# Kernel tuning notes

Measured on AMD Instinct MI355X. Metric: run time of the kernel, lower is better.

## Reference

```python
import jax, jax.numpy as jnp
import numpy as np

N = 8192
FEAT = 200
SEG = FEAT // 4  # 50
OUT = 300


def setup_inputs() -> dict:
    key = jax.random.key(0)
    ks = jax.random.split(key, 10)
    x = jax.random.normal(ks[0], (N, FEAT), dtype=jnp.float32)
    # row-normalized-ish dense adjacencies so activations stay O(1)
    A_S = jax.random.uniform(ks[1], (N, N), dtype=jnp.float32) / N
    A_F = jax.random.uniform(ks[2], (N, N), dtype=jnp.float32) / N
    gcn_W = jax.random.normal(ks[3], (SEG, SEG), dtype=jnp.float32) / np.sqrt(SEG)
    gcn_b = jnp.zeros((SEG,), dtype=jnp.float32)
    # 12 forget gates: order s1,s2,s3,f1,f2,f3,s1b,s2b,s3b,f1b,f2b,f3b
    gates_W = jax.random.normal(ks[4], (12, 2 * SEG, SEG), dtype=jnp.float32)
    gates_b = jax.random.normal(ks[5], (12, SEG), dtype=jnp.float32)
    proj_W = jax.random.normal(ks[6], (8 * SEG, OUT), dtype=jnp.float32) / np.sqrt(8 * SEG)
    proj_b = jnp.zeros((OUT,), dtype=jnp.float32)
    return {"x": x, "A_S": A_S, "A_F": A_F, "gcn_W": gcn_W, "gcn_b": gcn_b,
            "gates_W": gates_W, "gates_b": gates_b, "proj_W": proj_W, "proj_b": proj_b}


def _lgfm(x, A_S, A_F, gcn_W, gcn_b, gates_W, gates_b, proj_W, proj_b):
    seg = x.shape[1] // 4

    def gcn(h, A):
        # Kipf GraphConvolution: relu(A @ (h @ W) + b); dropout inactive (eval)
        return jax.nn.relu(A @ (h @ gcn_W) + gcn_b)

    def gate(i, h1, h2):
        a = jax.nn.sigmoid(jnp.concatenate([h1, h2], axis=1) @ gates_W[i] + gates_b[i])
        return a * h1

    GS1, GS2, GS3, GF1, GF2, GF3 = 0, 1, 2, 3, 4, 5
    GS1B, GS2B, GS3B, GF1B, GF2B, GF3B = 6, 7, 8, 9, 10, 11

    x1, x2, x3, x4 = x[:, :seg], x[:, seg:2 * seg], x[:, 2 * seg:3 * seg], x[:, 3 * seg:]

    # forward branch (F path then S gating)
    t1_XF1 = x1 + gcn(x1, A_F)
    t1_XS1 = gcn(x1, A_S)
    t1_XF2 = 0.2 * t1_XS1 + 0.8 * gcn(t1_XF1, A_F)
    t2_XF1 = x2 + gcn(x2, A_F)
    t2_XS1 = gcn(x2, A_S)
    t2_XS1 = t2_XS1 + gate(GS1, t1_XS1, t2_XS1)
    t2_XF2 = 0.2 * t2_XS1 + 0.8 * gcn(t2_XF1, A_F)
    t2_XF2 = gate(GF1, t1_XF2, t2_XF2) + t2_XF2
    t3_XF1 = 0.2 * x3 + 0.8 * gcn(x3, A_F)
    t3_XS1 = gcn(x3, A_S)
    t3_XS1 = t3_XS1 + gate(GS2, t2_XS1, t3_XS1)
    t3_XF2 = 0.2 * t3_XS1 + 0.8 * gcn(t3_XF1, A_F)
    t3_XF2 = gate(GF2, t2_XF2, t3_XF2) + t3_XF2
    t4_XF1 = x4 + gcn(x4, A_F)
    t4_XS1 = gcn(x4, A_S)
    t4_XS1 = t4_XS1 + gate(GS3, t3_XS1, t4_XS1)
    t4_XF2 = 0.2 * t4_XS1 + 0.8 * gcn(t4_XF1, A_F)
    t4_XF2 = gate(GF3, t3_XF2, t4_XF2) + t4_XF2

    # mirrored branch (S path then F gating)
    t1_XS1b = x1 + gcn(x1, A_S)
    t1_XF1b = gcn(x1, A_F)
    t1_XS2 = 0.2 * t1_XF1b + 0.8 * gcn(t1_XS1b, A_S)
    t2_XS1b = x2 + gcn(x2, A_S)
    t2_XF1b = gcn(x2, A_F)
    t2_XF1b = t2_XF1b + gate(GF1B, t1_XF1b, t2_XF1b)
    t2_XS2 = 0.2 * t2_XF1b + 0.8 * gcn(t2_XS1b, A_S)
    t2_XS2 = gate(GS1B, t1_XS2, t2_XS2) + t2_XS2
    t3_XS1b = 0.2 * x3 + 0.8 * gcn(x3, A_S)
    t3_XF1b = gcn(x3, A_F)
    t3_XF1b = t3_XF1b + gate(GF2B, t2_XF1b, t3_XF1b)
    t3_XS2 = 0.2 * t3_XF1b + 0.8 * gcn(t3_XS1b, A_S)
    t3_XS2 = gate(GS2B, t2_XS2, t3_XS2) + t3_XS2
    t4_XS1b = x4 + gcn(x4, A_S)
    t4_XF1b = gcn(x4, A_F)
    t4_XF1b = t4_XF1b + gate(GF3B, t3_XF1b, t4_XF1b)
    t4_XS2 = 0.2 * t4_XF1b + 0.8 * gcn(t4_XS1b, A_S)
    t4_XS2 = gate(GS3B, t3_XS2, t4_XS2) + t4_XS2

    h_L = jnp.concatenate([t1_XF2, t1_XS2, t2_XF2, t2_XS2,
                           t3_XF2, t3_XS2, t4_XF2, t4_XS2], axis=1)
    return h_L @ proj_W + proj_b


def reference(x, A_S, A_F, gcn_W, gcn_b, gates_W, gates_b, proj_W, proj_b):
    return _lgfm(x, A_S, A_F, gcn_W, gcn_b, gates_W, gates_b, proj_W, proj_b)
```

## Files before the change

kernel.cpp:

```cpp
#include <hip/hip_runtime.h>
#include <math.h>

typedef float float4v __attribute__((ext_vector_type(4)));
typedef __attribute__((ext_vector_type(4))) float f32x4;
typedef __attribute__((ext_vector_type(8))) short short8v;
typedef __attribute__((ext_vector_type(8))) unsigned short ushort8v;

#define NROW 8192
#define FEAT 200
#define OUTC 300
#define ZLD  256
#define HLK  448
#define HLN  384

__device__ __forceinline__ unsigned short f2bf(float x) {
  unsigned u = __float_as_uint(x);
  return (unsigned short)((u + 0x7fffu + ((u >> 16) & 1u)) >> 16);
}

__global__ __launch_bounds__(256) void zmul_t_kernel(
    const float* __restrict__ x, const float* __restrict__ W,
    unsigned short* __restrict__ Zt) {
  __shared__ float Ws[2500];
  __shared__ float hs[16][200];
  __shared__ float zbuf[16][256];
  int t = threadIdx.x;
  int r0 = blockIdx.x * 16;
  for (int i = t; i < 2500; i += 256) Ws[i] = W[i];
  for (int i = t; i < 16 * FEAT; i += 256)
    hs[0][i] = x[(size_t)r0 * FEAT + i];
  __syncthreads();
  for (int i = t; i < 16 * 256; i += 256) {
    int row = i >> 8, j = i & 255;
    float acc = 0.f;
    if (j < FEAT) {
      int s = j / 50, jj = j % 50;
      const float* hrow = &hs[row][s * 50];
      #pragma unroll 5
      for (int k = 0; k < 50; ++k) acc += hrow[k] * Ws[k * 50 + jj];
    }
    zbuf[row][j] = acc;
  }
  __syncthreads();
  unsigned int* Ztu = (unsigned int*)Zt;
  for (int i = t; i < 256 * 8; i += 256) {
    int j = i >> 3, w2 = i & 7;
    unsigned int lo = f2bf(zbuf[2 * w2][j]);
    unsigned int hi = f2bf(zbuf[2 * w2 + 1][j]);
    Ztu[((j * NROW + r0) >> 1) + w2] = lo | (hi << 16);
  }
}

__global__ __launch_bounds__(256, 2) void gemm_cvt_pair_kernel(
    const float* __restrict__ AF, const float* __restrict__ AS,
    const unsigned short* __restrict__ ZtF,
    const unsigned short* __restrict__ ZtS,
    float* __restrict__ Cpart) {
  int d = blockIdx.x;
  int L = (d & 7) * 64 + (d >> 3);
  int mat = L & 1;
  int ks  = (L >> 1) & 1;
  int cb  = (L >> 2) & 1;
  int rb  = L >> 3;

  const float* __restrict__ A = mat ? AS : AF;
  const unsigned short* __restrict__ Zt = mat ? ZtS : ZtF;

  int t = threadIdx.x;
  int lane = t & 63, wv = t >> 6;
  int row0 = rb * 128, n0 = cb * 128, k0 = ks * 4096;

  __shared__ short As[2][128 * 64];
  __shared__ short Bs[2][128 * 64];

  int srcAf[4], dstA[4];
  #pragma unroll
  for (int i = 0; i < 4; ++i) {
    int cc = i * 256 + t;
    int m = cc >> 3, s = cc & 7;
    srcAf[i] = (row0 + m) * NROW + s * 8;
    dstA[i] = m * 64 + ((s ^ (m & 7)) * 8);
  }
  int srcB[4], ldsDstB[4];
  #pragma unroll
  for (int i = 0; i < 4; ++i) {
    int c = i * 256 + t;
    int m = c >> 3, sl = c & 7;
    srcB[i] = (n0 + m) * NROW + ((sl ^ (m & 7)) * 8);
    ldsDstB[i] = (i * 256 + wv * 64) * 8;
  }

  f32x4 ar0[4], ar1[4];

#define STAGE_B(buf, kt)                                                              \
  {                                                                                   \
    _Pragma("unroll")                                                                 \
    for (int i = 0; i < 4; ++i)                                                       \
      __builtin_amdgcn_global_load_lds(                                               \
          (const __attribute__((address_space(1))) void*)(Zt + srcB[i] + (kt)),       \
          (__attribute__((address_space(3))) void*)(&Bs[buf][ldsDstB[i]]), 16, 0, 0); \
  }
#define LOAD_A(kt)                                         \
  {                                                        \
    _Pragma("unroll")                                      \
    for (int i = 0; i < 4; ++i) {                          \
      ar0[i] = *(const f32x4*)&A[srcAf[i] + (kt)];         \
      ar1[i] = *(const f32x4*)&A[srcAf[i] + (kt) + 4];     \
    }                                                      \
  }
#define WRITE_A(buf)                                                                    \
  {                                                                                     \
    _Pragma("unroll")                                                                   \
    for (int i = 0; i < 4; ++i) {                                                       \
      unsigned u0_, u1_, u2_, u3_;                                                      \
      asm("v_cvt_pk_bf16_f32 %0, %1, %2" : "=v"(u0_) : "v"(ar0[i][0]), "v"(ar0[i][1]));\
      asm("v_cvt_pk_bf16_f32 %0, %1, %2" : "=v"(u1_) : "v"(ar0[i][2]), "v"(ar0[i][3]));\
      asm("v_cvt_pk_bf16_f32 %0, %1, %2" : "=v"(u2_) : "v"(ar1[i][0]), "v"(ar1[i][1]));\
      asm("v_cvt_pk_bf16_f32 %0, %1, %2" : "=v"(u3_) : "v"(ar1[i][2]), "v"(ar1[i][3]));\
      union { unsigned u[4]; short8v v; } pk_;                                          \
      pk_.u[0] = u0_; pk_.u[1] = u1_; pk_.u[2] = u2_; pk_.u[3] = u3_;                   \
      *(short8v*)&As[buf][dstA[i]] = pk_.v;                                             \
    }                                                                                   \
  }

  f32x4 acc[4][4];
  #pragma unroll
  for (int i = 0; i < 4; ++i)
    #pragma unroll
    for (int j = 0; j < 4; ++j) acc[i][j] = (f32x4)0.f;

  int m0 = (wv >> 1) * 64, n0w = (wv & 1) * 64;
  int l15 = lane & 15, l4 = lane >> 4;

  int cur = 0;
  LOAD_A(k0)
  STAGE_B(0, k0)
  WRITE_A(0)
  __syncthreads();

  for (int it = 0; it < 64; ++it) {
    if (it + 1 < 64) {
      STAGE_B(cur ^ 1, k0 + (it + 1) * 64)
      LOAD_A(k0 + (it + 1) * 64)
    }

    #pragma unroll
    for (int kk = 0; kk < 2; ++kk) {
      int slot = kk * 4 + l4;
      short8v a[4], b[4];
      #pragma unroll
      for (int i = 0; i < 4; ++i) {
        int m = m0 + i * 16 + l15;
        a[i] = *(const short8v*)&As[cur][m * 64 + ((slot ^ (m & 7)) * 8)];
        int n = n0w + i * 16 + l15;
        b[i] = *(const short8v*)&Bs[cur][n * 64 + ((slot ^ (n & 7)) * 8)];
      }
      #pragma unroll
      for (int i = 0; i < 4; ++i)
        #pragma unroll
        for (int j = 0; j < 4; ++j)
          acc[i][j] = __builtin_amdgcn_mfma_f32_16x16x32_bf16(a[i], b[j], acc[i][j], 0, 0, 0);
    }

    if (it + 1 < 64) WRITE_A(cur ^ 1)
    __syncthreads();
    cur ^= 1;
  }
#undef STAGE_B
#undef LOAD_A
#undef WRITE_A

  int s = mat * 2 + ks;
  #pragma unroll
  for (int i = 0; i < 4; ++i) {
    #pragma unroll
    for (int j = 0; j < 4; ++j) {
      int c = n0 + n0w + j * 16 + l15;
      #pragma unroll
      for (int q = 0; q < 4; ++q) {
        int r = row0 + m0 + i * 16 + l4 * 4 + q;
        Cpart[((size_t)(s * NROW + r) << 8) + c] = acc[i][j][q];
      }
    }
  }
}

__global__ __launch_bounds__(256) void reduce_zmul_kernel(
    const float* __restrict__ Cpart, const float* __restrict__ bias,
    const float* __restrict__ x, const float* __restrict__ W,
    float* __restrict__ GF0, float* __restrict__ GS0,
    unsigned short* __restrict__ ZtF, unsigned short* __restrict__ ZtS) {
  __shared__ float Ws[2500];
  __shared__ float hs[16][200];
  __shared__ float zbuf[16][256];
  int t = threadIdx.x;
  int r0 = blockIdx.x * 16;
  int w = t >> 6, j = t & 63;
  bool act = j < 50;
  int rbase = r0 + w * 4;
  for (int i = t; i < 2500; i += 256) Ws[i] = W[i];

  const float alpha[4] = {1.f, 1.f, 0.2f, 1.f};
  const float beta[4]  = {1.f, 1.f, 0.8f, 1.f};
  float gf[4][4], gs[4][4];
  if (act) {
    float bv = bias[j];
    #pragma unroll
    for (int r = 0; r < 4; ++r)
      #pragma unroll
      for (int s = 0; s < 4; ++s) {
        int c = s * 50 + j;
        size_t base = (((size_t)(rbase + r)) << 8) + c;
        float vF = Cpart[base] + Cpart[base + (size_t)NROW * 256];
        float vS = Cpart[base + (size_t)2 * NROW * 256] + Cpart[base + (size_t)3 * NROW * 256];
        gf[r][s] = fmaxf(vF + bv, 0.f);
        gs[r][s] = fmaxf(vS + bv, 0.f);
        GF0[(size_t)(rbase + r) * FEAT + c] = gf[r][s];
        GS0[(size_t)(rbase + r) * FEAT + c] = gs[r][s];
      }
    #pragma unroll
    for (int r = 0; r < 4; ++r)
      #pragma unroll
      for (int s = 0; s < 4; ++s)
        hs[w * 4 + r][s * 50 + j] =
            alpha[s] * x[(size_t)(rbase + r) * FEAT + s * 50 + j] + beta[s] * gf[r][s];
  }
  __syncthreads();
  for (int i = t; i < 16 * 256; i += 256) {
    int row = i >> 8, jj = i & 255;
    float acc = 0.f;
    if (jj < FEAT) {
      int s = jj / 50, j2 = jj % 50;
      const float* hrow = &hs[row][s * 50];
      #pragma unroll 5
      for (int k = 0; k < 50; ++k) acc += hrow[k] * Ws[k * 50 + j2];
    }
    zbuf[row][jj] = acc;
  }
  __syncthreads();
  {
    unsigned int* Ztu = (unsigned int*)ZtF;
    for (int i = t; i < 256 * 8; i += 256) {
      int j2 = i >> 3, w2 = i & 7;
      unsigned int lo = f2bf(zbuf[2 * w2][j2]);
      unsigned int hi = f2bf(zbuf[2 * w2 + 1][j2]);
      Ztu[((j2 * NROW + r0) >> 1) + w2] = lo | (hi << 16);
    }
  }
  if (act) {
    #pragma unroll
    for (int r = 0; r < 4; ++r)
      #pragma unroll
      for (int s = 0; s < 4; ++s)
        hs[w * 4 + r][s * 50 + j] =
            alpha[s] * x[(size_t)(rbase + r) * FEAT + s * 50 + j] + beta[s] * gs[r][s];
  }
  __syncthreads();
  for (int i = t; i < 16 * 256; i += 256) {
    int row = i >> 8, jj = i & 255;
    float acc = 0.f;
    if (jj < FEAT) {
      int s = jj / 50, j2 = jj % 50;
      const float* hrow = &hs[row][s * 50];
      #pragma unroll 5
      for (int k = 0; k < 50; ++k) acc += hrow[k] * Ws[k * 50 + j2];
    }
    zbuf[row][jj] = acc;
  }
  __syncthreads();
  {
    unsigned int* Ztu = (unsigned int*)ZtS;
    for (int i = t; i < 256 * 8; i += 256) {
      int j2 = i >> 3, w2 = i & 7;
      unsigned int lo = f2bf(zbuf[2 * w2][j2]);
      unsigned int hi = f2bf(zbuf[2 * w2 + 1][j2]);
      Ztu[((j2 * NROW + r0) >> 1) + w2] = lo | (hi << 16);
    }
  }
}

__device__ __forceinline__ void gate4(const float* __restrict__ gWi, const float* __restrict__ gbi,
                                      float* hsw, float* Wg, int t, int j, bool act,
                                      const float* h1, const float* h2, float* aout) {
  if (act) {
    #pragma unroll
    for (int r = 0; r < 4; ++r) { hsw[r * 128 + j] = h1[r]; hsw[r * 128 + 64 + j] = h2[r]; }
  }
  {
    const float4v* src = (const float4v*)gWi;
    float4v* dst = (float4v*)Wg;
    #pragma unroll
    for (int u = 0; u < 5; ++u) {
      int i = t + 256 * u;
      if (i < 1250) dst[i] = src[i];
    }
  }
  __syncthreads();
  float acc0 = 0.f, acc1 = 0.f, acc2 = 0.f, acc3 = 0.f;
  if (act) {
    float bv = gbi[j];
    acc0 = bv; acc1 = bv; acc2 = bv; acc3 = bv;
    #pragma unroll 2
    for (int k = 0; k < 50; ++k) {
      float wv = Wg[k * 50 + j];
      acc0 += hsw[0 * 128 + k] * wv;
      acc1 += hsw[1 * 128 + k] * wv;
      acc2 += hsw[2 * 128 + k] * wv;
      acc3 += hsw[3 * 128 + k] * wv;
    }
    #pragma unroll 2
    for (int k = 0; k < 50; ++k) {
      float wv = Wg[(50 + k) * 50 + j];
      acc0 += hsw[0 * 128 + 64 + k] * wv;
      acc1 += hsw[1 * 128 + 64 + k] * wv;
      acc2 += hsw[2 * 128 + 64 + k] * wv;
      acc3 += hsw[3 * 128 + 64 + k] * wv;
    }
  }
  __syncthreads();
  float accs[4] = {acc0, acc1, acc2, acc3};
  #pragma unroll
  for (int r = 0; r < 4; ++r) {
    float a = 1.f / (1.f + expf(-accs[r]));
    aout[r] = a * h1[r];
  }
}

__global__ __launch_bounds__(256) void reduce_chain_kernel(
    const float* __restrict__ Cpart, const float* __restrict__ bias,
    const float* __restrict__ GF0, const float* __restrict__ GS0,
    const float* __restrict__ gW, const float* __restrict__ gb,
    unsigned short* __restrict__ hLb) {
  __shared__ float hsb[4 * 512];
  __shared__ float Wg[5000];
  int t = threadIdx.x;
  int w = t >> 6, j = t & 63;
  bool act = j < 50;
  float* hsw = &hsb[w * 512];
  int rbase = blockIdx.x * 16 + w * 4;

  float gf0[4][4], gs0[4][4], gf1[4][4], gs1[4][4];
  if (act) {
    float bv = bias[j];
    #pragma unroll
    for (int r = 0; r < 4; ++r)
      #pragma unroll
      for (int s = 0; s < 4; ++s) {
        int c = s * 50 + j;
        size_t base = (((size_t)(rbase + r)) << 8) + c;
        float vF = Cpart[base] + Cpart[base + (size_t)NROW * 256];
        float vS = Cpart[base + (size_t)2 * NROW * 256] + Cpart[base + (size_t)3 * NROW * 256];
        gf1[r][s] = fmaxf(vF + bv, 0.f);
        gs1[r][s] = fmaxf(vS + bv, 0.f);
        gf0[r][s] = GF0[(size_t)(rbase + r) * FEAT + c];
        gs0[r][s] = GS0[(size_t)(rbase + r) * FEAT + c];
      }
  }
  if (!act) {
    for (int p = j - 50; p < 48; p += 14)
      #pragma unroll
      for (int r = 0; r < 4; ++r)
        hLb[(size_t)(rbase + r) * HLK + 400 + p] = 0;
  }

  float xf2[4], xs1[4], pre[4], a[4], h1t[4], h2t[4];
  #pragma unroll
  for (int r = 0; r < 4; ++r) xf2[r] = 0.2f * gs0[r][0] + 0.8f * gf1[r][0];
  if (act) {
    #pragma unroll
    for (int r = 0; r < 4; ++r) hLb[(size_t)(rbase + r) * HLK + 0 + j] = f2bf(xf2[r]);
  }
  #pragma unroll
  for (int r = 0; r < 4; ++r) { h1t[r] = gs0[r][0]; h2t[r] = gs0[r][1]; }
  gate4(gW + 0 * 5000, gb + 0 * 50, hsw, Wg, t, j, act, h1t, h2t, a);
  #pragma unroll
  for (int r = 0; r < 4; ++r) xs1[r] = gs0[r][1] + a[r];
  #pragma unroll
  for (int r = 0; r < 4; ++r) pre[r] = 0.2f * xs1[r] + 0.8f * gf1[r][1];
  gate4(gW + 3 * 5000, gb + 3 * 50, hsw, Wg, t, j, act, xf2, pre, a);
  #pragma unroll
  for (int r = 0; r < 4; ++r) xf2[r] = a[r] + pre[r];
  if (act) {
    #pragma unroll
    for (int r = 0; r < 4; ++r) hLb[(size_t)(rbase + r) * HLK + 100 + j] = f2bf(xf2[r]);
  }
  #pragma unroll
  for (int r = 0; r < 4; ++r) { h1t[r] = xs1[r]; h2t[r] = gs0[r][2]; }
  gate4(gW + 1 * 5000, gb + 1 * 50, hsw, Wg, t, j, act, h1t, h2t, a);
  #pragma unroll
  for (int r = 0; r < 4; ++r) xs1[r] = gs0[r][2] + a[r];
  #pragma unroll
  for (int r = 0; r < 4; ++r) pre[r] = 0.2f * xs1[r] + 0.8f * gf1[r][2];
  gate4(gW + 4 * 5000, gb + 4 * 50, hsw, Wg, t, j, act, xf2, pre, a);
  #pragma unroll
  for (int r = 0; r < 4; ++r) xf2[r] = a[r] + pre[r];
  if (act) {
    #pragma unroll
    for (int r = 0; r < 4; ++r) hLb[(size_t)(rbase + r) * HLK + 200 + j] = f2bf(xf2[r]);
  }
  #pragma unroll
  for (int r = 0; r < 4; ++r) { h1t[r] = xs1[r]; h2t[r] = gs0[r][3]; }
  gate4(gW + 2 * 5000, gb + 2 * 50, hsw, Wg, t, j, act, h1t, h2t, a);
  #pragma unroll
  for (int r = 0; r < 4; ++r) xs1[r] = gs0[r][3] + a[r];
  #pragma unroll
  for (int r = 0; r < 4; ++r) pre[r] = 0.2f * xs1[r] + 0.8f * gf1[r][3];
  gate4(gW + 5 * 5000, gb + 5 * 50, hsw, Wg, t, j, act, xf2, pre, a);
  #pragma unroll
  for (int r = 0; r < 4; ++r) xf2[r] = a[r] + pre[r];
  if (act) {
    #pragma unroll
    for (int r = 0; r < 4; ++r) hLb[(size_t)(rbase + r) * HLK + 300 + j] = f2bf(xf2[r]);
  }

  float xs2[4], xf1b[4];
  #pragma unroll
  for (int r = 0; r < 4; ++r) xs2[r] = 0.2f * gf0[r][0] + 0.8f * gs1[r][0];
  if (act) {
    #pragma unroll
    for (int r = 0; r < 4; ++r) hLb[(size_t)(rbase + r) * HLK + 50 + j] = f2bf(xs2[r]);
  }
  #pragma unroll
  for (int r = 0; r < 4; ++r) { h1t[r] = gf0[r][0]; h2t[r] = gf0[r][1]; }
  gate4(gW + 9 * 5000, gb + 9 * 50, hsw, Wg, t, j, act, h1t, h2t, a);
  #pragma unroll
  for (int r = 0; r < 4; ++r) xf1b[r] = gf0[r][1] + a[r];
  #pragma unroll
  for (int r = 0; r < 4; ++r) pre[r] = 0.2f * xf1b[r] + 0.8f * gs1[r][1];
  gate4(gW + 6 * 5000, gb + 6 * 50, hsw, Wg, t, j, act, xs2, pre, a);
  #pragma unroll
  for (int r = 0; r < 4; ++r) xs2[r] = a[r] + pre[r];
  if (act) {
    #pragma unroll
    for (int r = 0; r < 4; ++r) hLb[(size_t)(rbase + r) * HLK + 150 + j] = f2bf(xs2[r]);
  }
  #pragma unroll
  for (int r = 0; r < 4; ++r) { h1t[r] = xf1b[r]; h2t[r] = gf0[r][2]; }
  gate4(gW + 10 * 5000, gb + 10 * 50, hsw, Wg, t, j, act, h1t, h2t, a);
  #pragma unroll
  for (int r = 0; r < 4; ++r) xf1b[r] = gf0[r][2] + a[r];
  #pragma unroll
  for (int r = 0; r < 4; ++r) pre[r] = 0.2f * xf1b[r] + 0.8f * gs1[r][2];
  gate4(gW + 7 * 5000, gb + 7 * 50, hsw, Wg, t, j, act, xs2, pre, a);
  #pragma unroll
  for (int r = 0; r < 4; ++r) xs2[r] = a[r] + pre[r];
  if (act) {
    #pragma unroll
    for (int r = 0; r < 4; ++r) hLb[(size_t)(rbase + r) * HLK + 250 + j] = f2bf(xs2[r]);
  }
  #pragma unroll
  for (int r = 0; r < 4; ++r) { h1t[r] = xf1b[r]; h2t[r] = gf0[r][3]; }
  gate4(gW + 11 * 5000, gb + 11 * 50, hsw, Wg, t, j, act, h1t, h2t, a);
  #pragma unroll
  for (int r = 0; r < 4; ++r) xf1b[r] = gf0[r][3] + a[r];
  #pragma unroll
  for (int r = 0; r < 4; ++r) pre[r] = 0.2f * xf1b[r] + 0.8f * gs1[r][3];
  gate4(gW + 8 * 5000, gb + 8 * 50, hsw, Wg, t, j, act, xs2, pre, a);
  #pragma unroll
  for (int r = 0; r < 4; ++r) xs2[r] = a[r] + pre[r];
  if (act) {
    #pragma unroll
    for (int r = 0; r < 4; ++r) hLb[(size_t)(rbase + r) * HLK + 350 + j] = f2bf(xs2[r]);
  }
}

__global__ __launch_bounds__(256) void wconv_kernel(
    const float* __restrict__ pW, unsigned short* __restrict__ Wtb) {
  int i = blockIdx.x * 256 + threadIdx.x;
  if (i >= HLN * HLK) return;
  int n = i / HLK, k = i % HLK;
  float v = (n < OUTC && k < 400) ? pW[k * OUTC + n] : 0.f;
  Wtb[i] = f2bf(v);
}

__global__ __launch_bounds__(256, 2) void proj_gemm_kernel(
    const unsigned short* __restrict__ hLb,
    const unsigned short* __restrict__ Wtb,
    const float* __restrict__ pb, float* __restrict__ outp) {
  int d = blockIdx.x;
  int L = (d & 7) * 24 + (d >> 3);
  int rb = L / 3, cb = L % 3;

  int t = threadIdx.x;
  int lane = t & 63, wv = t >> 6;
  int row0 = rb * 128, n0 = cb * 128;

  __shared__ short As[2][128 * 64];
  __shared__ short Bs[2][128 * 64];

  int srcA[4], srcB[4], ldsDst[4];
  #pragma unroll
  for (int i = 0; i < 4; ++i) {
    int c = i * 256 + t;
    int m = c >> 3, sl = c & 7;
    int sw = ((sl ^ (m & 7)) * 8);
    srcA[i] = (row0 + m) * HLK + sw;
    srcB[i] = (n0 + m) * HLK + sw;
    ldsDst[i] = (i * 256 + wv * 64) * 8;
  }

#define STAGE_TILE(buf, kt)                                                          \
  {                                                                                  \
    _Pragma("unroll")                                                                \
    for (int i = 0; i < 4; ++i) {                                                    \
      __builtin_amdgcn_global_load_lds(                                              \
          (const __attribute__((address_space(1))) void*)(hLb + srcA[i] + (kt)),     \
          (__attribute__((address_space(3))) void*)(&As[buf][ldsDst[i]]), 16, 0, 0); \
      __builtin_amdgcn_global_load_lds(                                              \
          (const __attribute__((address_space(1))) void*)(Wtb + srcB[i] + (kt)),     \
          (__attribute__((address_space(3))) void*)(&Bs[buf][ldsDst[i]]), 16, 0, 0); \
    }                                                                                \
  }

  f32x4 acc[4][4];
  #pragma unroll
  for (int i = 0; i < 4; ++i)
    #pragma unroll
    for (int j = 0; j < 4; ++j) acc[i][j] = (f32x4)0.f;

  int m0 = (wv >> 1) * 64, n0w = (wv & 1) * 64;
  int l15 = lane & 15, l4 = lane >> 4;

  int cur = 0;
  STAGE_TILE(0, 0)
  __syncthreads();

  for (int it = 0; it < 7; ++it) {
    if (it + 1 < 7) STAGE_TILE(cur ^ 1, (it + 1) * 64)

    #pragma unroll
    for (int kk = 0; kk < 2; ++kk) {
      int slot = kk * 4 + l4;
      short8v a[4], b[4];
      #pragma unroll
      for (int i = 0; i < 4; ++i) {
        int m = m0 + i * 16 + l15;
        a[i] = *(const short8v*)&As[cur][m * 64 + ((slot ^ (m & 7)) * 8)];
        int n = n0w + i * 16 + l15;
        b[i] = *(const short8v*)&Bs[cur][n * 64 + ((slot ^ (n & 7)) * 8)];
      }
      #pragma unroll
      for (int i = 0; i < 4; ++i)
        #pragma unroll
        for (int j = 0; j < 4; ++j)
          acc[i][j] = __builtin_amdgcn_mfma_f32_16x16x32_bf16(a[i], b[j], acc[i][j], 0, 0, 0);
    }
    __syncthreads();
    cur ^= 1;
  }
#undef STAGE_TILE

  #pragma unroll
  for (int i = 0; i < 4; ++i) {
    #pragma unroll
    for (int j = 0; j < 4; ++j) {
      int c = n0 + n0w + j * 16 + l15;
      if (c < OUTC) {
        float b = pb[c];
        #pragma unroll
        for (int q = 0; q < 4; ++q) {
          int r = row0 + m0 + i * 16 + l4 * 4 + q;
          outp[(size_t)r * OUTC + c] = acc[i][j][q] + b;
        }
      }
    }
  }
}

__global__ __launch_bounds__(256) void zmul_f32_kernel(
    const float* __restrict__ x, const float* __restrict__ g,
    const float* __restrict__ W,
    float a0, float a1, float a2, float a3,
    float b0, float b1, float b2, float b3,
    float* __restrict__ Zp) {
  __shared__ float Ws[2500];
  __shared__ float hs[200];
  int t = threadIdx.x;
  for (int i = t; i < 2500; i += 256) Ws[i] = W[i];
  float alpha[4] = {a0, a1, a2, a3};
  float beta[4]  = {b0, b1, b2, b3};
  int s  = (t < 200) ? (t / 50) : 0;
  int jj = (t < 200) ? (t % 50) : 0;
  int r0 = blockIdx.x * 32;
  for (int rr = 0; rr < 32; ++rr) {
    int row = r0 + rr;
    __syncthreads();
    if (t < 200) hs[t] = alpha[s] * x[row * FEAT + t] + beta[s] * g[row * FEAT + t];
    __syncthreads();
    float acc = 0.f;
    if (t < 200) {
      const float* hrow = &hs[s * 50];
      #pragma unroll 5
      for (int k = 0; k < 50; ++k) acc += hrow[k] * Ws[k * 50 + jj];
    }
    Zp[row * ZLD + t] = (t < 200) ? acc : 0.f;
  }
}

#define BM 64
#define BN 64
#define BK 32
#define ALD 68
__global__ __launch_bounds__(256) void gemm_relu_kernel(
    const float* __restrict__ A, const float* __restrict__ Zp,
    const float* __restrict__ bias, float* __restrict__ C) {
  int wg  = blockIdx.x;
  int swz = (wg & 7) * 64 + (wg >> 3);
  int rb  = swz >> 2;
  int cb  = swz & 3;
  int t   = threadIdx.x;
  int rt  = t >> 4, ct = t & 15;
  __shared__ __align__(16) float As[BK][ALD];
  __shared__ __align__(16) float Zs[BK][BN];
  float acc[4][4];
  #pragma unroll
  for (int i = 0; i < 4; ++i)
    #pragma unroll
    for (int j = 0; j < 4; ++j) acc[i][j] = 0.f;
  const int row0 = rb * BM, col0 = cb * BN;
  int ar = t >> 3;
  int ak = (t & 7) * 4;
  int zr = t >> 4;
  int zc = (t & 15) * 4;
  const float4v* A4 = (const float4v*)A;
  const float4v* Z4 = (const float4v*)Zp;
  float4v a0, a1, z0, z1;
  a0 = A4[((size_t)(row0 + ar) * NROW + 0 + ak) >> 2];
  a1 = A4[((size_t)(row0 + ar + 32) * NROW + 0 + ak) >> 2];
  z0 = Z4[((0 + zr) * ZLD + col0 + zc) >> 2];
  z1 = Z4[((0 + zr + 16) * ZLD + col0 + zc) >> 2];
  for (int kt = 0; kt < NROW; kt += BK) {
    __syncthreads();
    #pragma unroll
    for (int u = 0; u < 4; ++u) As[ak + u][ar] = a0[u];
    #pragma unroll
    for (int u = 0; u < 4; ++u) As[ak + u][ar + 32] = a1[u];
    *(float4v*)&Zs[zr][zc]      = z0;
    *(float4v*)&Zs[zr + 16][zc] = z1;
    __syncthreads();
    int kn = kt + BK;
    if (kn < NROW) {
      a0 = A4[((size_t)(row0 + ar) * NROW + kn + ak) >> 2];
      a1 = A4[((size_t)(row0 + ar + 32) * NROW + kn + ak) >> 2];
      z0 = Z4[((kn + zr) * ZLD + col0 + zc) >> 2];
      z1 = Z4[((kn + zr + 16) * ZLD + col0 + zc) >> 2];
    }
    #pragma unroll
    for (int k = 0; k < BK; ++k) {
      float4v av = *(const float4v*)&As[k][rt * 4];
      float4v zv = *(const float4v*)&Zs[k][ct * 4];
      #pragma unroll
      for (int i = 0; i < 4; ++i)
        #pragma unroll
        for (int j = 0; j < 4; ++j) acc[i][j] += av[i] * zv[j];
    }
  }
  #pragma unroll
  for (int i = 0; i < 4; ++i) {
    int grow = row0 + rt * 4 + i;
    #pragma unroll
    for (int j = 0; j < 4; ++j) {
      int gcol = col0 + ct * 4 + j;
      if (gcol < FEAT) {
        float v = acc[i][j] + bias[gcol % 50];
        C[(size_t)grow * FEAT + gcol] = fmaxf(v, 0.f);
      }
    }
  }
}

__global__ __launch_bounds__(256) void chain_top_kernel(
    const float* __restrict__ GS0, const float* __restrict__ GF1,
    const float* __restrict__ gW, const float* __restrict__ gb,
    unsigned short* __restrict__ hLb) {
  __shared__ float hsb[4 * 512];
  __shared__ float Wg[5000];
  int t = threadIdx.x;
  int w = t >> 6, j = t & 63;
  bool act = j < 50;
  float* hsw = &hsb[w * 512];
  int rbase = blockIdx.x * 16 + w * 4;
  float gs[4][4], gf[4][4];
  #pragma unroll
  for (int r = 0; r < 4; ++r)
    #pragma unroll
    for (int s = 0; s < 4; ++s) { gs[r][s] = 0.f; gf[r][s] = 0.f; }
  if (act) {
    #pragma unroll
    for (int r = 0; r < 4; ++r)
      #pragma unroll
      for (int s = 0; s < 4; ++s) {
        gs[r][s] = GS0[(size_t)(rbase + r) * FEAT + s * 50 + j];
        gf[r][s] = GF1[(size_t)(rbase + r) * FEAT + s * 50 + j];
      }
  }
  float xf2[4], xs1[4], pre[4], a[4], h1t[4], h2t[4];
  #pragma unroll
  for (int r = 0; r < 4; ++r) xf2[r] = 0.2f * gs[r][0] + 0.8f * gf[r][0];
  if (act) {
    #pragma unroll
    for (int r = 0; r < 4; ++r) hLb[(size_t)(rbase + r) * HLK + 0 + j] = f2bf(xf2[r]);
  }
  #pragma unroll
  for (int r = 0; r < 4; ++r) { h1t[r] = gs[r][0]; h2t[r] = gs[r][1]; }
  gate4(gW + 0 * 5000, gb + 0 * 50, hsw, Wg, t, j, act, h1t, h2t, a);
  #pragma unroll
  for (int r = 0; r < 4; ++r) xs1[r] = gs[r][1] + a[r];
  #pragma unroll
  for (int r = 0; r < 4; ++r) pre[r] = 0.2f * xs1[r] + 0.8f * gf[r][1];
  gate4(gW + 3 * 5000, gb + 3 * 50, hsw, Wg, t, j, act, xf2, pre, a);
  #pragma unroll
  for (int r = 0; r < 4; ++r) xf2[r] = a[r] + pre[r];
  if (act) {
    #pragma unroll
    for (int r = 0; r < 4; ++r) hLb[(size_t)(rbase + r) * HLK + 100 + j] = f2bf(xf2[r]);
  }
  #pragma unroll
  for (int r = 0; r < 4; ++r) { h1t[r] = xs1[r]; h2t[r] = gs[r][2]; }
  gate4(gW + 1 * 5000, gb + 1 * 50, hsw, Wg, t, j, act, h1t, h2t, a);
  #pragma unroll
  for (int r = 0; r < 4; ++r) xs1[r] = gs[r][2] + a[r];
  #pragma unroll
  for (int r = 0; r < 4; ++r) pre[r] = 0.2f * xs1[r] + 0.8f * gf[r][2];
  gate4(gW + 4 * 5000, gb + 4 * 50, hsw, Wg, t, j, act, xf2, pre, a);
  #pragma unroll
  for (int r = 0; r < 4; ++r) xf2[r] = a[r] + pre[r];
  if (act) {
    #pragma unroll
    for (int r = 0; r < 4; ++r) hLb[(size_t)(rbase + r) * HLK + 200 + j] = f2bf(xf2[r]);
  }
  #pragma unroll
  for (int r = 0; r < 4; ++r) { h1t[r] = xs1[r]; h2t[r] = gs[r][3]; }
  gate4(gW + 2 * 5000, gb + 2 * 50, hsw, Wg, t, j, act, h1t, h2t, a);
  #pragma unroll
  for (int r = 0; r < 4; ++r) xs1[r] = gs[r][3] + a[r];
  #pragma unroll
  for (int r = 0; r < 4; ++r) pre[r] = 0.2f * xs1[r] + 0.8f * gf[r][3];
  gate4(gW + 5 * 5000, gb + 5 * 50, hsw, Wg, t, j, act, xf2, pre, a);
  #pragma unroll
  for (int r = 0; r < 4; ++r) xf2[r] = a[r] + pre[r];
  if (act) {
    #pragma unroll
    for (int r = 0; r < 4; ++r) hLb[(size_t)(rbase + r) * HLK + 300 + j] = f2bf(xf2[r]);
  }
}

__global__ __launch_bounds__(256) void chain_bottom_kernel(
    const float* __restrict__ GF0, const float* __restrict__ GS1,
    const float* __restrict__ gW, const float* __restrict__ gb,
    unsigned short* __restrict__ hLb) {
  __shared__ float hsb[4 * 512];
  __shared__ float Wg[5000];
  int t = threadIdx.x;
  int w = t >> 6, j = t & 63;
  bool act = j < 50;
  float* hsw = &hsb[w * 512];
  int rbase = blockIdx.x * 16 + w * 4;
  float gf0[4][4], gs1[4][4];
  #pragma unroll
  for (int r = 0; r < 4; ++r)
    #pragma unroll
    for (int s = 0; s < 4; ++s) { gf0[r][s] = 0.f; gs1[r][s] = 0.f; }
  if (act) {
    #pragma unroll
    for (int r = 0; r < 4; ++r)
      #pragma unroll
      for (int s = 0; s < 4; ++s) {
        gf0[r][s] = GF0[(size_t)(rbase + r) * FEAT + s * 50 + j];
        gs1[r][s] = GS1[(size_t)(rbase + r) * FEAT + s * 50 + j];
      }
  }
  float xs2[4], xf1b[4], pre[4], a[4], h1t[4], h2t[4];
  #pragma unroll
  for (int r = 0; r < 4; ++r) xs2[r] = 0.2f * gf0[r][0] + 0.8f * gs1[r][0];
  if (act) {
    #pragma unroll
    for (int r = 0; r < 4; ++r) hLb[(size_t)(rbase + r) * HLK + 50 + j] = f2bf(xs2[r]);
  }
  #pragma unroll
  for (int r = 0; r < 4; ++r) { h1t[r] = gf0[r][0]; h2t[r] = gf0[r][1]; }
  gate4(gW + 9 * 5000, gb + 9 * 50, hsw, Wg, t, j, act, h1t, h2t, a);
  #pragma unroll
  for (int r = 0; r < 4; ++r) xf1b[r] = gf0[r][1] + a[r];
  #pragma unroll
  for (int r = 0; r < 4; ++r) pre[r] = 0.2f * xf1b[r] + 0.8f * gs1[r][1];
  gate4(gW + 6 * 5000, gb + 6 * 50, hsw, Wg, t, j, act, xs2, pre, a);
  #pragma unroll
  for (int r = 0; r < 4; ++r) xs2[r] = a[r] + pre[r];
  if (act) {
    #pragma unroll
    for (int r = 0; r < 4; ++r) hLb[(size_t)(rbase + r) * HLK + 150 + j] = f2bf(xs2[r]);
  }
  #pragma unroll
  for (int r = 0; r < 4; ++r) { h1t[r] = xf1b[r]; h2t[r] = gf0[r][2]; }
  gate4(gW + 10 * 5000, gb + 10 * 50, hsw, Wg, t, j, act, h1t, h2t, a);
  #pragma unroll
  for (int r = 0; r < 4; ++r) xf1b[r] = gf0[r][2] + a[r];
  #pragma unroll
  for (int r = 0; r < 4; ++r) pre[r] = 0.2f * xf1b[r] + 0.8f * gs1[r][2];
  gate4(gW + 7 * 5000, gb + 7 * 50, hsw, Wg, t, j, act, xs2, pre, a);
  #pragma unroll
  for (int r = 0; r < 4; ++r) xs2[r] = a[r] + pre[r];
  if (act) {
    #pragma unroll
    for (int r = 0; r < 4; ++r) hLb[(size_t)(rbase + r) * HLK + 250 + j] = f2bf(xs2[r]);
  }
  #pragma unroll
  for (int r = 0; r < 4; ++r) { h1t[r] = xf1b[r]; h2t[r] = gf0[r][3]; }
  gate4(gW + 11 * 5000, gb + 11 * 50, hsw, Wg, t, j, act, h1t, h2t, a);
  #pragma unroll
  for (int r = 0; r < 4; ++r) xf1b[r] = gf0[r][3] + a[r];
  #pragma unroll
  for (int r = 0; r < 4; ++r) pre[r] = 0.2f * xf1b[r] + 0.8f * gs1[r][3];
  gate4(gW + 8 * 5000, gb + 8 * 50, hsw, Wg, t, j, act, xs2, pre, a);
  #pragma unroll
  for (int r = 0; r < 4; ++r) xs2[r] = a[r] + pre[r];
  if (act) {
    #pragma unroll
    for (int r = 0; r < 4; ++r) hLb[(size_t)(rbase + r) * HLK + 350 + j] = f2bf(xs2[r]);
  }
}

extern "C" void kernel_launch(void* const* d_in, const int* in_sizes, int n_in,
                              void* d_out, int out_size, void* d_ws, size_t ws_size,
                              hipStream_t stream) {
  const float* x       = (const float*)d_in[0];
  const float* A_S     = (const float*)d_in[1];
  const float* A_F     = (const float*)d_in[2];
  const float* gcn_W   = (const float*)d_in[3];
  const float* gcn_b   = (const float*)d_in[4];
  const float* gates_W = (const float*)d_in[5];
  const float* gates_b = (const float*)d_in[6];
  const float* proj_W  = (const float*)d_in[7];
  const float* proj_b  = (const float*)d_in[8];
  float* out = (float*)d_out;

  const size_t szZt    = (size_t)256 * NROW * 2;
  const size_t szCpart = (size_t)4 * NROW * 256 * 4;
  const size_t szG     = (size_t)NROW * FEAT * 4;
  const size_t szHLb   = (size_t)NROW * HLK * 2;
  const size_t szWtb   = (size_t)HLN * HLK * 2;
  const size_t need = 3 * szZt + szCpart + 2 * szG + szHLb + szWtb;

  if (ws_size >= need) {
    char* w = (char*)d_ws;
    unsigned short* Zt0  = (unsigned short*)w;           w += szZt;
    unsigned short* Zt1F = (unsigned short*)w;           w += szZt;
    unsigned short* Zt1S = (unsigned short*)w;           w += szZt;
    float* Cpart = (float*)w;                            w += szCpart;
    float* GF0 = (float*)w;                              w += szG;
    float* GS0 = (float*)w;                              w += szG;
    unsigned short* hLb = (unsigned short*)w;            w += szHLb;
    unsigned short* Wtb = (unsigned short*)w;

    wconv_kernel<<<(HLN * HLK + 255) / 256, 256, 0, stream>>>(proj_W, Wtb);
    zmul_t_kernel<<<512, 256, 0, stream>>>(x, gcn_W, Zt0);

    gemm_cvt_pair_kernel<<<512, 256, 0, stream>>>(A_F, A_S, Zt0, Zt0, Cpart);
    reduce_zmul_kernel<<<512, 256, 0, stream>>>(Cpart, gcn_b, x, gcn_W, GF0, GS0, Zt1F, Zt1S);

    gemm_cvt_pair_kernel<<<512, 256, 0, stream>>>(A_F, A_S, Zt1F, Zt1S, Cpart);
    reduce_chain_kernel<<<512, 256, 0, stream>>>(Cpart, gcn_b, GF0, GS0, gates_W, gates_b, hLb);

    proj_gemm_kernel<<<192, 256, 0, stream>>>(hLb, Wtb, proj_b, out);
  } else {
    char* w = (char*)d_ws;
    float* Z   = (float*)w;                              w += (size_t)NROW * ZLD * 4;
    float* GF0 = (float*)w;                              w += szG;
    float* GS0 = (float*)w;                              w += szG;
    float* GF1 = (float*)w;                              w += szG;
    float* GS1 = (float*)w;                              w += szG;
    unsigned short* hLb = (unsigned short*)w;            w += szHLb;
    unsigned short* Wtb = (unsigned short*)w;

    hipMemsetAsync(hLb, 0, szHLb, stream);
    wconv_kernel<<<(HLN * HLK + 255) / 256, 256, 0, stream>>>(proj_W, Wtb);

    zmul_f32_kernel<<<256, 256, 0, stream>>>(x, x, gcn_W, 1.f, 1.f, 1.f, 1.f, 0.f, 0.f, 0.f, 0.f, Z);
    gemm_relu_kernel<<<512, 256, 0, stream>>>(A_F, Z, gcn_b, GF0);
    gemm_relu_kernel<<<512, 256, 0, stream>>>(A_S, Z, gcn_b, GS0);
    zmul_f32_kernel<<<256, 256, 0, stream>>>(x, GF0, gcn_W, 1.f, 1.f, 0.2f, 1.f, 1.f, 1.f, 0.8f, 1.f, Z);
    gemm_relu_kernel<<<512, 256, 0, stream>>>(A_F, Z, gcn_b, GF1);
    zmul_f32_kernel<<<256, 256, 0, stream>>>(x, GS0, gcn_W, 1.f, 1.f, 0.2f, 1.f, 1.f, 1.f, 0.8f, 1.f, Z);
    gemm_relu_kernel<<<512, 256, 0, stream>>>(A_S, Z, gcn_b, GS1);

    chain_top_kernel<<<512, 256, 0, stream>>>(GS0, GF1, gates_W, gates_b, hLb);
    chain_bottom_kernel<<<512, 256, 0, stream>>>(GF0, GS1, gates_W, gates_b, hLb);
    proj_gemm_kernel<<<192, 256, 0, stream>>>(hLb, Wtb, proj_b, out);
  }
}
```

Baseline: 486.1 us.

## Spill bf16 adjacency copies in first GEMM pass and reuse in second

The first adjacency GEMM now writes its bf16-converted A tiles back to global workspace (only from column-block 0 blocks), and the second GEMM reads those bf16 copies with direct global-to-LDS loads instead of re-reading and converting the fp32 adjacencies. The aim is to halve the dominant memory traffic of the second pass (2 bytes instead of 4 per element) and drop its conversion work. In exchange, the first pass writes an extra 256 MB, and a much larger workspace is required. If the workspace is too small, execution falls back to the older path.

```diff
diff --git a/kernel.cpp b/kernel.cpp
--- a/kernel.cpp
+++ b/kernel.cpp
@@ -51,11 +51,12 @@
   }
 }
 
-__global__ __launch_bounds__(256, 2) void gemm_cvt_pair_kernel(
+__global__ __launch_bounds__(256, 2) void gemm_cvt_spill_kernel(
     const float* __restrict__ AF, const float* __restrict__ AS,
     const unsigned short* __restrict__ ZtF,
     const unsigned short* __restrict__ ZtS,
-    float* __restrict__ Cpart) {
+    float* __restrict__ Cpart,
+    unsigned short* __restrict__ AbF_o, unsigned short* __restrict__ AbS_o) {
   int d = blockIdx.x;
   int L = (d & 7) * 64 + (d >> 3);
   int mat = L & 1;
@@ -65,6 +66,7 @@
 
   const float* __restrict__ A = mat ? AS : AF;
   const unsigned short* __restrict__ Zt = mat ? ZtS : ZtF;
+  unsigned short* __restrict__ Abo = mat ? AbS_o : AbF_o;
 
   int t = threadIdx.x;
   int lane = t & 63, wv = t >> 6;
@@ -108,7 +110,7 @@
       ar1[i] = *(const f32x4*)&A[srcAf[i] + (kt) + 4];     \
     }                                                      \
   }
-#define WRITE_A(buf)                                                                    \
+#define WRITE_A(buf, kt)                                                                \
   {                                                                                     \
     _Pragma("unroll")                                                                   \
     for (int i = 0; i < 4; ++i) {                                                       \
@@ -120,6 +122,7 @@
       union { unsigned u[4]; short8v v; } pk_;                                          \
       pk_.u[0] = u0_; pk_.u[1] = u1_; pk_.u[2] = u2_; pk_.u[3] = u3_;                   \
       *(short8v*)&As[buf][dstA[i]] = pk_.v;                                             \
+      if (cb == 0) *(short8v*)&Abo[(size_t)srcAf[i] + (kt)] = pk_.v;                    \
     }                                                                                   \
   }
 
@@ -135,7 +138,7 @@
   int cur = 0;
   LOAD_A(k0)
   STAGE_B(0, k0)
-  WRITE_A(0)
+  WRITE_A(0, k0)
   __syncthreads();
 
   for (int it = 0; it < 64; ++it) {
@@ -162,13 +165,113 @@
           acc[i][j] = __builtin_amdgcn_mfma_f32_16x16x32_bf16(a[i], b[j], acc[i][j], 0, 0, 0);
     }
 
-    if (it + 1 < 64) WRITE_A(cur ^ 1)
+    if (it + 1 < 64) WRITE_A(cur ^ 1, k0 + (it + 1) * 64)
     __syncthreads();
     cur ^= 1;
   }
 #undef STAGE_B
 #undef LOAD_A
 #undef WRITE_A
+
+  int s = mat * 2 + ks;
+  #pragma unroll
+  for (int i = 0; i < 4; ++i) {
+    #pragma unroll
+    for (int j = 0; j < 4; ++j) {
+      int c = n0 + n0w + j * 16 + l15;
+      #pragma unroll
+      for (int q = 0; q < 4; ++q) {
+        int r = row0 + m0 + i * 16 + l4 * 4 + q;
+        Cpart[((size_t)(s * NROW + r) << 8) + c] = acc[i][j][q];
+      }
+    }
+  }
+}
+
+__global__ __launch_bounds__(256, 2) void gemm_pair_kernel(
+    const unsigned short* __restrict__ AbF,
+    const unsigned short* __restrict__ AbS,
+    const unsigned short* __restrict__ ZtF,
+    const unsigned short* __restrict__ ZtS,
+    float* __restrict__ Cpart) {
+  int d = blockIdx.x;
+  int L = (d & 7) * 64 + (d >> 3);
+  int mat = L & 1;
+  int ks  = (L >> 1) & 1;
+  int cb  = (L >> 2) & 1;
+  int rb  = L >> 3;
+
+  const unsigned short* __restrict__ Ab = mat ? AbS : AbF;
+  const unsigned short* __restrict__ Zt = mat ? ZtS : ZtF;
+
+  int t = threadIdx.x;
+  int lane = t & 63, wv = t >> 6;
+  int row0 = rb * 128, n0 = cb * 128, k0 = ks * 4096;
+
+  __shared__ short As[2][128 * 64];
+  __shared__ short Bs[2][128 * 64];
+
+  int srcA[4], srcB[4], ldsDst[4];
+  #pragma unroll
+  for (int i = 0; i < 4; ++i) {
+    int c = i * 256 + t;
+    int m = c >> 3, sl = c & 7;
+    int sw = ((sl ^ (m & 7)) * 8);
+    srcA[i] = (row0 + m) * NROW + sw;
+    srcB[i] = (n0 + m) * NROW + sw;
+    ldsDst[i] = (i * 256 + wv * 64) * 8;
+  }
+
+#define STAGE_TILE(buf, kt)                                                          \
+  {                                                                                  \
+    _Pragma("unroll")                                                                \
+    for (int i = 0; i < 4; ++i) {                                                    \
+      __builtin_amdgcn_global_load_lds(                                              \
+          (const __attribute__((address_space(1))) void*)(Ab + srcA[i] + (kt)),      \
+          (__attribute__((address_space(3))) void*)(&As[buf][ldsDst[i]]), 16, 0, 0); \
+      __builtin_amdgcn_global_load_lds(                                              \
+          (const __attribute__((address_space(1))) void*)(Zt + srcB[i] + (kt)),      \
+          (__attribute__((address_space(3))) void*)(&Bs[buf][ldsDst[i]]), 16, 0, 0); \
+    }                                                                                \
+  }
+
+  f32x4 acc[4][4];
+  #pragma unroll
+  for (int i = 0; i < 4; ++i)
+    #pragma unroll
+    for (int j = 0; j < 4; ++j) acc[i][j] = (f32x4)0.f;
+
+  int m0 = (wv >> 1) * 64, n0w = (wv & 1) * 64;
+  int l15 = lane & 15, l4 = lane >> 4;
+
+  int cur = 0;
+  STAGE_TILE(0, k0)
+  __syncthreads();
+
+  for (int it = 0; it < 64; ++it) {
+    if (it + 1 < 64) STAGE_TILE(cur ^ 1, k0 + (it + 1) * 64)
+
+    #pragma unroll
+    for (int kk = 0; kk < 2; ++kk) {
+      int slot = kk * 4 + l4;
+      short8v a[4], b[4];
+      #pragma unroll
+      for (int i = 0; i < 4; ++i) {
+        int m = m0 + i * 16 + l15;
+        a[i] = *(const short8v*)&As[cur][m * 64 + ((slot ^ (m & 7)) * 8)];
+        int n = n0w + i * 16 + l15;
+        b[i] = *(const short8v*)&Bs[cur][n * 64 + ((slot ^ (n & 7)) * 8)];
+      }
+      #pragma unroll
+      for (int i = 0; i < 4; ++i)
+        #pragma unroll
+        for (int j = 0; j < 4; ++j)
+          acc[i][j] = __builtin_amdgcn_mfma_f32_16x16x32_bf16(a[i], b[j], acc[i][j], 0, 0, 0);
+    }
+    __syncthreads();
+    cur ^= 1;
+  }
+#undef STAGE_TILE
 
   int s = mat * 2 + ks;
   #pragma unroll
@@ -835,15 +938,18 @@
   const float* proj_b  = (const float*)d_in[8];
   float* out = (float*)d_out;
 
+  const size_t szAb    = (size_t)NROW * NROW * 2;
   const size_t szZt    = (size_t)256 * NROW * 2;
   const size_t szCpart = (size_t)4 * NROW * 256 * 4;
   const size_t szG     = (size_t)NROW * FEAT * 4;
   const size_t szHLb   = (size_t)NROW * HLK * 2;
   const size_t szWtb   = (size_t)HLN * HLK * 2;
-  const size_t need = 3 * szZt + szCpart + 2 * szG + szHLb + szWtb;
+  const size_t need = 2 * szAb + 3 * szZt + szCpart + 2 * szG + szHLb + szWtb;
 
   if (ws_size >= need) {
     char* w = (char*)d_ws;
+    unsigned short* AbF  = (unsigned short*)w;           w += szAb;
+    unsigned short* AbS  = (unsigned short*)w;           w += szAb;
     unsigned short* Zt0  = (unsigned short*)w;           w += szZt;
     unsigned short* Zt1F = (unsigned short*)w;           w += szZt;
     unsigned short* Zt1S = (unsigned short*)w;           w += szZt;
@@ -856,10 +962,10 @@
     wconv_kernel<<<(HLN * HLK + 255) / 256, 256, 0, stream>>>(proj_W, Wtb);
     zmul_t_kernel<<<512, 256, 0, stream>>>(x, gcn_W, Zt0);
 
-    gemm_cvt_pair_kernel<<<512, 256, 0, stream>>>(A_F, A_S, Zt0, Zt0, Cpart);
+    gemm_cvt_spill_kernel<<<512, 256, 0, stream>>>(A_F, A_S, Zt0, Zt0, Cpart, AbF, AbS);
     reduce_zmul_kernel<<<512, 256, 0, stream>>>(Cpart, gcn_b, x, gcn_W, GF0, GS0, Zt1F, Zt1S);
 
-    gemm_cvt_pair_kernel<<<512, 256, 0, stream>>>(A_F, A_S, Zt1F, Zt1S, Cpart);
+    gemm_pair_kernel<<<512, 256, 0, stream>>>(AbF, AbS, Zt1F, Zt1S, Cpart);
     reduce_chain_kernel<<<512, 256, 0, stream>>>(Cpart, gcn_b, GF0, GS0, gates_W, gates_b, hLb);
 
     proj_gemm_kernel<<<192, 256, 0, stream>>>(hLb, Wtb, proj_b, out);
```

New measurement: 481.3 us. No clear change (-1.0%).
